# Kernel optimization log

Measured on AMD Instinct MI355X. Metric: run time of the kernel, lower is better.

## Reference

```python
import jax, jax.numpy as jnp
import numpy as np

IN_FEATURES = 2048
HIDDEN_DIM = 1024
ENC_DIM = 1024
DEC_DIM = IN_FEATURES - ENC_DIM
MASK_VAL = -50000.0


def setup_inputs() -> dict:
    key = jax.random.key(0)
    k1, k2, k3, k4, k5 = jax.random.split(key, 5)
    B, S = 32, 2048
    encoder_outputs = jax.random.normal(k1, (B, S, ENC_DIM), dtype=jnp.float32)
    decoder_state = jax.random.normal(k2, (B, DEC_DIM), dtype=jnp.float32)
    # lengths in [1, S]
    sequence_length = jax.random.randint(k3, (B,), 1, S + 1).astype(jnp.int64)
    # fc_w: Linear(in_features, hidden_dim, bias=False) -> weight [hidden, in_feat]
    W = jax.random.normal(k4, (HIDDEN_DIM, IN_FEATURES), dtype=jnp.float32) / np.sqrt(IN_FEATURES)
    # fc_v: Linear(hidden_dim, 1, bias=False) -> weight [1, hidden]; store as [hidden]
    v = jax.random.normal(k5, (HIDDEN_DIM,), dtype=jnp.float32) / np.sqrt(HIDDEN_DIM)
    return {"encoder_outputs": encoder_outputs, "sequence_length": sequence_length,
            "decoder_state": decoder_state, "W": W, "v": v}


def reference(encoder_outputs, sequence_length, decoder_state, W, v):
    # score = v^T tanh(W [h; s]) == v^T tanh(W_enc h + W_dec s)  (avoids concat)
    W_enc = W[:, :ENC_DIM]      # [H, De]
    W_dec = W[:, ENC_DIM:]      # [H, Dd]
    # [B, S, H] + [B, 1, H]
    hidden = jnp.tanh(jnp.einsum('bse,he->bsh', encoder_outputs, W_enc)
                      + jnp.einsum('bd,hd->bh', decoder_state, W_dec)[:, None, :])
    logits = jnp.einsum('bsh,h->bs', hidden, v)                      # [B, S]
    S = logits.shape[1]
    mask = jnp.arange(S)[None, :] < sequence_length[:, None]          # [B, S]
    masked_logits = jnp.where(mask, logits, jnp.float32(MASK_VAL))
    attn_weight = jax.nn.softmax(masked_logits, axis=1)               # [B, S]
    out = jnp.einsum('bs,bse->be', attn_weight, encoder_outputs)      # [B, De]
    return (out, attn_weight)
```

## Files before the change

kernel.cpp:

```cpp
#include <hip/hip_runtime.h>
#include <hip/hip_bf16.h>

#define B 32
#define S 2048
#define E 1024
#define H 1024
#define MASK_VAL -50000.0f

typedef __attribute__((ext_vector_type(8))) short bf16x8_t;
typedef __attribute__((ext_vector_type(4))) float f32x4_t;

__device__ __forceinline__ float fast_tanh(float x) {
    float a = fabsf(x);
    float e = __expf(-2.0f * a);
    float t = (1.0f - e) / (1.0f + e);
    return copysignf(t, x);
}

__device__ __forceinline__ float b2f(short s) {
    return __uint_as_float(((unsigned)(unsigned short)s) << 16);
}

__device__ __forceinline__ bf16x8_t cvt8(const float4 f0, const float4 f1) {
    union { bf16x8_t s8; __hip_bfloat162 h[4]; } u;
    u.h[0] = __float22bfloat162_rn(make_float2(f0.x, f0.y));
    u.h[1] = __float22bfloat162_rn(make_float2(f0.z, f0.w));
    u.h[2] = __float22bfloat162_rn(make_float2(f1.x, f1.y));
    u.h[3] = __float22bfloat162_rn(make_float2(f1.z, f1.w));
    return u.s8;
}

__device__ __forceinline__ void gload16(const void* g, void* l) {
    __builtin_amdgcn_global_load_lds(
        (const __attribute__((address_space(1))) void*)g,
        (__attribute__((address_space(3))) void*)l, 16, 0, 0);
}

__global__ __launch_bounds__(256) void kprep(
    const float* __restrict__ W, const float* __restrict__ dec,
    __hip_bfloat16* __restrict__ Wb, float* __restrict__ dec_proj)
{
    int blk = blockIdx.x, tid = threadIdx.x;
    if (blk < 1024) {
        int idx = (blk * 256 + tid) * 4;
        int h = idx >> 10, e = idx & 1023;
        float4 f = *(const float4*)(W + (size_t)h * 2048 + e);
        __hip_bfloat162 p0 = __float22bfloat162_rn(make_float2(f.x, f.y));
        __hip_bfloat162 p1 = __float22bfloat162_rn(make_float2(f.z, f.w));
        *reinterpret_cast<__hip_bfloat162*>(Wb + idx)     = p0;
        *reinterpret_cast<__hip_bfloat162*>(Wb + idx + 2) = p1;
    } else {
        int gid = (blk - 1024) * 256 + tid;
        int b = gid >> 10, h = gid & 1023;
        const float4* wd = (const float4*)(W + (size_t)h * 2048 + 1024);
        const float4* dd = (const float4*)(dec + b * 1024);
        float acc = 0.f;
        for (int d = 0; d < 256; ++d) {
            float4 w4 = wd[d], d4 = dd[d];
            acc += w4.x * d4.x + w4.y * d4.y + w4.z * d4.z + w4.w * d4.w;
        }
        dec_proj[gid] = acc;
    }
}

__global__ __launch_bounds__(256) void k0_encconv(
    const float* __restrict__ enc, const int* __restrict__ seq,
    __hip_bfloat16* __restrict__ encb)
{
    int c = blockIdx.x, b = blockIdx.y;
    if (c * 128 >= seq[b]) return;
    size_t base = ((size_t)b * S + c * 128) * E;
    const float* src = enc + base;
    __hip_bfloat16* dst = encb + base;
    int tid = threadIdx.x;
    #pragma unroll 4
    for (int it = 0; it < 64; ++it) {
        int idx = it * 2048 + tid * 8;
        float4 f0 = *(const float4*)(src + idx);
        float4 f1 = *(const float4*)(src + idx + 4);
        *(bf16x8_t*)(dst + idx) = cvt8(f0, f1);
    }
}

template<int AMODE>
__global__ __launch_bounds__(256, 2) void k2_mfma(
    const float* __restrict__ enc, const __hip_bfloat16* __restrict__ encb,
    const __hip_bfloat16* __restrict__ Wb, const float* __restrict__ v,
    const float* __restrict__ dec_proj, const int* __restrict__ seq,
    float* __restrict__ part)
{
    const int bid  = blockIdx.x;
    const int pair = (bid >> 6) * 8 + (bid & 7);
    const int ht   = (bid >> 3) & 7;
    const int b    = pair >> 4;
    const int s0   = (pair & 15) * 128;
    if (s0 >= seq[b]) return;
    const int h0 = ht * 128;

    const int tid  = threadIdx.x;
    const int wave = tid >> 6;
    const int lane = tid & 63;
    const int wr = wave >> 1, wc = wave & 1;
    const int cr = lane & 15, cg = lane >> 4;

    __shared__ __hip_bfloat16 Al[2][128 * 64];
    __shared__ __hip_bfloat16 Bl[2][128 * 64];

    const int colb  = (tid & 7) * 16;
    const int rbase = tid >> 3;

    f32x4_t acc[4][4];
    #pragma unroll
    for (int m = 0; m < 4; ++m)
        #pragma unroll
        for (int n = 0; n < 4; ++n)
            acc[m][n] = (f32x4_t){0.f, 0.f, 0.f, 0.f};

    auto stage = [&](int buf, int kt) {
        #pragma unroll
        for (int i = 0; i < 4; ++i) {
            const int row   = i * 32 + rbase;
            const int scolb = colb ^ ((row & 7) << 4);
            const __hip_bfloat16* bg =
                Wb + (((size_t)(h0 + row)) << 10) + kt * 64 + (scolb >> 1);
            gload16(bg, (char*)&Bl[buf][0] + (i * 256 + tid) * 16);
            if (AMODE == 0) {
                const __hip_bfloat16* ag =
                    encb + (((size_t)b * S + s0 + row) << 10) + kt * 64 + (scolb >> 1);
                gload16(ag, (char*)&Al[buf][0] + (i * 256 + tid) * 16);
            } else {
                const float* af =
                    enc + (((size_t)b * S + s0 + row) << 10) + kt * 64 + (tid & 7) * 8;
                bf16x8_t v8 = cvt8(*(const float4*)af, *(const float4*)(af + 4));
                *(bf16x8_t*)((char*)&Al[buf][0] + row * 128 + scolb) = v8;
            }
        }
    };

    stage(0, 0);
    __syncthreads();
    int cur = 0;
    for (int kt = 0; kt < 16; ++kt) {
        if (kt < 15) stage(cur ^ 1, kt + 1);
        bf16x8_t afr[2][4], bfr[2][4];
        #pragma unroll
        for (int ks = 0; ks < 2; ++ks) {
            #pragma unroll
            for (int m = 0; m < 4; ++m) {
                const int arow  = wr * 64 + m * 16 + cr;
                const int acolb = (ks * 64 + cg * 16) ^ ((arow & 7) << 4);
                afr[ks][m] = *(const bf16x8_t*)((const char*)&Al[cur][0] + arow * 128 + acolb);
                const int brow  = wc * 64 + m * 16 + cr;
                const int bcolb = (ks * 64 + cg * 16) ^ ((brow & 7) << 4);
                bfr[ks][m] = *(const bf16x8_t*)((const char*)&Bl[cur][0] + brow * 128 + bcolb);
            }
        }
        #pragma unroll
        for (int ks = 0; ks < 2; ++ks)
            #pragma unroll
            for (int m = 0; m < 4; ++m)
                #pragma unroll
                for (int n = 0; n < 4; ++n)
                    acc[m][n] = __builtin_amdgcn_mfma_f32_16x16x32_bf16(
                        afr[ks][m], bfr[ks][n], acc[m][n], 0, 0, 0);
        __syncthreads();
        cur ^= 1;
    }

    float vv[4], dp[4];
    #pragma unroll
    for (int n = 0; n < 4; ++n) {
        int h = h0 + wc * 64 + n * 16 + cr;
        vv[n] = v[h];
        dp[n] = dec_proj[b * H + h];
    }
    #pragma unroll
    for (int m = 0; m < 4; ++m) {
        #pragma unroll
        for (int j = 0; j < 4; ++j) {
            float t = 0.f;
            #pragma unroll
            for (int n = 0; n < 4; ++n)
                t += vv[n] * fast_tanh(acc[m][n][j] + dp[n]);
            t += __shfl_xor(t, 1);
            t += __shfl_xor(t, 2);
            t += __shfl_xor(t, 4);
            t += __shfl_xor(t, 8);
            if (cr == 0) {
                int srow = s0 + wr * 64 + m * 16 + cg * 4 + j;
                part[(size_t)(b * S + srow) * 16 + ht * 2 + wc] = t;
            }
        }
    }
}

__global__ __launch_bounds__(256) void k3_softmax(
    const float* __restrict__ part, const int* __restrict__ seq,
    float* __restrict__ attn)
{
    int b = blockIdx.x, tid = threadIdx.x;
    int len = seq[b];
    float vals[8];
    float mx = -3.4e38f;
    #pragma unroll
    for (int i = 0; i < 8; ++i) {
        int s = i * 256 + tid;
        float x = MASK_VAL;
        if (s < len) {
            const f32x4_t* p = (const f32x4_t*)&part[(size_t)(b * S + s) * 16];
            f32x4_t a = p[0], c = p[1], d = p[2], e = p[3];
            x = (a[0] + a[1] + a[2] + a[3]) + (c[0] + c[1] + c[2] + c[3]) +
                (d[0] + d[1] + d[2] + d[3]) + (e[0] + e[1] + e[2] + e[3]);
        }
        vals[i] = x;
        mx = fmaxf(mx, x);
    }
    #pragma unroll
    for (int off = 1; off < 64; off <<= 1) mx = fmaxf(mx, __shfl_xor(mx, off));
    __shared__ float red[8];
    int wave = tid >> 6, lane = tid & 63;
    if (lane == 0) red[wave] = mx;
    __syncthreads();
    mx = fmaxf(fmaxf(red[0], red[1]), fmaxf(red[2], red[3]));
    float e[8];
    float sum = 0.f;
    #pragma unroll
    for (int i = 0; i < 8; ++i) { e[i] = __expf(vals[i] - mx); sum += e[i]; }
    #pragma unroll
    for (int off = 1; off < 64; off <<= 1) sum += __shfl_xor(sum, off);
    if (lane == 0) red[4 + wave] = sum;
    __syncthreads();
    sum = red[4] + red[5] + red[6] + red[7];
    float inv = 1.0f / sum;
    #pragma unroll
    for (int i = 0; i < 8; ++i) attn[b * S + i * 256 + tid] = e[i] * inv;
}

template<int AMODE>
__global__ __launch_bounds__(256) void k4_partial(
    const float* __restrict__ enc, const __hip_bfloat16* __restrict__ encb,
    const float* __restrict__ attn, const int* __restrict__ seq,
    float* __restrict__ opart)
{
    int c = blockIdx.x, b = blockIdx.y, tid = threadIdx.x;
    int base_s = c * 256;
    int len = seq[b];
    if (AMODE == 0) {
        int e0 = (tid & 127) * 8;
        int so = tid >> 7;
        float av[8];
        #pragma unroll
        for (int j = 0; j < 8; ++j) av[j] = 0.f;
        if (base_s < len) {
            int s_end = min(256, len - base_s);
            for (int s = so; s < s_end; s += 2) {
                float w = attn[b * S + base_s + s];
                bf16x8_t u = *(const bf16x8_t*)(encb +
                    (((size_t)b * S + base_s + s) << 10) + e0);
                #pragma unroll
                for (int j = 0; j < 8; ++j) av[j] += w * b2f(u[j]);
            }
        }
        float* dst = opart + (((size_t)(b * 8 + c) * 2 + so) << 10) + e0;
        *(float4*)dst       = make_float4(av[0], av[1], av[2], av[3]);
        *(float4*)(dst + 4) = make_float4(av[4], av[5], av[6], av[7]);
    } else {
        float4 acc = make_float4(0.f, 0.f, 0.f, 0.f);
        if (base_s < len) {
            int s_end = min(256, len - base_s);
            const float* ep = enc + ((size_t)b * S + base_s) * E + (tid & 255) * 4;
            const float* ap = attn + b * S + base_s;
            for (int s = 0; s < s_end; ++s) {
                float w = ap[s];
                float4 ev = *(const float4*)ep;
                ep += E;
                acc.x += w * ev.x; acc.y += w * ev.y;
                acc.z += w * ev.z; acc.w += w * ev.w;
            }
        }
        float* dst = opart + (((size_t)(b * 8 + c) * 2) << 10) + tid * 4;
        *(float4*)dst = acc;
        float* dst2 = opart + (((size_t)(b * 8 + c) * 2 + 1) << 10) + tid * 4;
        *(float4*)dst2 = make_float4(0.f, 0.f, 0.f, 0.f);
    }
}

__global__ __launch_bounds__(256) void k5_reduce(
    const float* __restrict__ opart, float* __restrict__ out)
{
    int gid = blockIdx.x * 256 + threadIdx.x;
    int b = gid >> 10, e = gid & 1023;
    float s = 0.f;
    #pragma unroll
    for (int c = 0; c < 16; ++c) s += opart[((size_t)(b * 16 + c) << 10) + e];
    out[gid] = s;
}

extern "C" void kernel_launch(void* const* d_in, const int* in_sizes, int n_in,
                              void* d_out, int out_size, void* d_ws, size_t ws_size,
                              hipStream_t stream)
{
    const float* enc = (const float*)d_in[0];
    const int*   seq = (const int*)d_in[1];
    const float* dec = (const float*)d_in[2];
    const float* W   = (const float*)d_in[3];
    const float* v   = (const float*)d_in[4];

    float* out  = (float*)d_out;
    float* attn = out + B * E;

    float* dec_proj = (float*)d_ws;
    float* part     = dec_proj + B * H;
    float* opart    = part + (size_t)B * S * 16;
    __hip_bfloat16* Wb = (__hip_bfloat16*)(opart + (size_t)B * 16 * 1024);
    __hip_bfloat16* encb = Wb + (size_t)H * E;

    const size_t need = (size_t)(B * H + B * S * 16 + B * 16 * 1024) * 4
                      + (size_t)H * E * 2 + (size_t)B * S * E * 2;
    const bool use_encb = ws_size >= need;

    hipLaunchKernelGGL(kprep, dim3(1024 + 128), dim3(256), 0, stream,
                       W, dec, Wb, dec_proj);
    if (use_encb) {
        hipLaunchKernelGGL(k0_encconv, dim3(S / 128, B), dim3(256), 0, stream,
                           enc, seq, encb);
        hipLaunchKernelGGL(k2_mfma<0>, dim3(4096), dim3(256), 0, stream,
                           enc, encb, Wb, v, dec_proj, seq, part);
    } else {
        hipLaunchKernelGGL(k2_mfma<1>, dim3(4096), dim3(256), 0, stream,
                           enc, encb, Wb, v, dec_proj, seq, part);
    }
    hipLaunchKernelGGL(k3_softmax, dim3(B), dim3(256), 0, stream,
                       part, seq, attn);
    if (use_encb) {
        hipLaunchKernelGGL(k4_partial<0>, dim3(8, B), dim3(256), 0, stream,
                           enc, encb, attn, seq, opart);
    } else {
        hipLaunchKernelGGL(k4_partial<1>, dim3(8, B), dim3(256), 0, stream,
                           enc, encb, attn, seq, opart);
    }
    hipLaunchKernelGGL(k5_reduce, dim3(B * E / 256), dim3(256), 0, stream,
                       opart, out);
}
```

Before: 265.2 us.

## Enlarge MFMA score tile to 256x256 with 512 threads and fuse enc conversion into prep

The score GEMM moves from 128x128 tiles with 256 threads to 256x256 tiles with 512 threads (8 waves, each computing 128x64). This raises operand reuse per LDS load and cuts global traffic for W and enc. The enc-to-bf16 conversion kernel is folded into the prep kernel to save a launch. In exchange, LDS use doubles to 128KB per block, accumulator register pressure rises, and the coarser 256-row sequence granularity skips fewer masked rows.

```diff
diff --git a/kernel.cpp b/kernel.cpp
--- a/kernel.cpp
+++ b/kernel.cpp
@@ -38,7 +38,9 @@
 
 __global__ __launch_bounds__(256) void kprep(
     const float* __restrict__ W, const float* __restrict__ dec,
-    __hip_bfloat16* __restrict__ Wb, float* __restrict__ dec_proj)
+    const float* __restrict__ enc, const int* __restrict__ seq,
+    __hip_bfloat16* __restrict__ Wb, float* __restrict__ dec_proj,
+    __hip_bfloat16* __restrict__ encb)
 {
     int blk = blockIdx.x, tid = threadIdx.x;
     if (blk < 1024) {
@@ -49,7 +51,7 @@
         __hip_bfloat162 p1 = __float22bfloat162_rn(make_float2(f.z, f.w));
         *reinterpret_cast<__hip_bfloat162*>(Wb + idx)     = p0;
         *reinterpret_cast<__hip_bfloat162*>(Wb + idx + 2) = p1;
-    } else {
+    } else if (blk < 1152) {
         int gid = (blk - 1024) * 256 + tid;
         int b = gid >> 10, h = gid & 1023;
         const float4* wd = (const float4*)(W + (size_t)h * 2048 + 1024);
@@ -60,58 +62,56 @@
             acc += w4.x * d4.x + w4.y * d4.y + w4.z * d4.z + w4.w * d4.w;
         }
         dec_proj[gid] = acc;
-    }
-}
-
-__global__ __launch_bounds__(256) void k0_encconv(
-    const float* __restrict__ enc, const int* __restrict__ seq,
-    __hip_bfloat16* __restrict__ encb)
-{
-    int c = blockIdx.x, b = blockIdx.y;
-    if (c * 128 >= seq[b]) return;
-    size_t base = ((size_t)b * S + c * 128) * E;
-    const float* src = enc + base;
-    __hip_bfloat16* dst = encb + base;
-    int tid = threadIdx.x;
-    #pragma unroll 4
-    for (int it = 0; it < 64; ++it) {
-        int idx = it * 2048 + tid * 8;
-        float4 f0 = *(const float4*)(src + idx);
-        float4 f1 = *(const float4*)(src + idx + 4);
-        *(bf16x8_t*)(dst + idx) = cvt8(f0, f1);
+    } else {
+        int g = blk - 1152;
+        int c = g & 15, b = g >> 4;
+        if (c * 128 >= seq[b]) return;
+        size_t base = ((size_t)b * S + c * 128) * E;
+        const float* src = enc + base;
+        __hip_bfloat16* dst = encb + base;
+        #pragma unroll 4
+        for (int it = 0; it < 64; ++it) {
+            int idx = it * 2048 + tid * 8;
+            float4 f0 = *(const float4*)(src + idx);
+            float4 f1 = *(const float4*)(src + idx + 4);
+            *(bf16x8_t*)(dst + idx) = cvt8(f0, f1);
+        }
     }
 }
 
 template<int AMODE>
-__global__ __launch_bounds__(256, 2) void k2_mfma(
+__global__ __launch_bounds__(512, 2) void k2_mfma(
     const float* __restrict__ enc, const __hip_bfloat16* __restrict__ encb,
     const __hip_bfloat16* __restrict__ Wb, const float* __restrict__ v,
     const float* __restrict__ dec_proj, const int* __restrict__ seq,
     float* __restrict__ part)
 {
-    const int bid  = blockIdx.x;
-    const int pair = (bid >> 6) * 8 + (bid & 7);
-    const int ht   = (bid >> 3) & 7;
-    const int b    = pair >> 4;
-    const int s0   = (pair & 15) * 128;
+    const int bid = blockIdx.x;
+    const int xcd = bid & 7;
+    const int q   = bid >> 3;
+    const int nt  = q & 3;
+    const int p   = (q >> 2) * 8 + xcd;
+    const int b   = p >> 3;
+    const int st  = p & 7;
+    const int s0  = st * 256;
     if (s0 >= seq[b]) return;
-    const int h0 = ht * 128;
+    const int h0 = nt * 256;
 
     const int tid  = threadIdx.x;
     const int wave = tid >> 6;
     const int lane = tid & 63;
-    const int wr = wave >> 1, wc = wave & 1;
+    const int wr = wave >> 2, wc = wave & 3;
     const int cr = lane & 15, cg = lane >> 4;
 
-    __shared__ __hip_bfloat16 Al[2][128 * 64];
-    __shared__ __hip_bfloat16 Bl[2][128 * 64];
+    __shared__ __hip_bfloat16 Al[2][256 * 64];
+    __shared__ __hip_bfloat16 Bl[2][256 * 64];
 
     const int colb  = (tid & 7) * 16;
     const int rbase = tid >> 3;
 
-    f32x4_t acc[4][4];
-    #pragma unroll
-    for (int m = 0; m < 4; ++m)
+    f32x4_t acc[8][4];
+    #pragma unroll
+    for (int m = 0; m < 8; ++m)
         #pragma unroll
         for (int n = 0; n < 4; ++n)
             acc[m][n] = (f32x4_t){0.f, 0.f, 0.f, 0.f};
@@ -119,15 +119,15 @@
     auto stage = [&](int buf, int kt) {
         #pragma unroll
         for (int i = 0; i < 4; ++i) {
-            const int row   = i * 32 + rbase;
+            const int row   = i * 64 + rbase;
             const int scolb = colb ^ ((row & 7) << 4);
             const __hip_bfloat16* bg =
                 Wb + (((size_t)(h0 + row)) << 10) + kt * 64 + (scolb >> 1);
-            gload16(bg, (char*)&Bl[buf][0] + (i * 256 + tid) * 16);
+            gload16(bg, (char*)&Bl[buf][0] + (i * 512 + tid) * 16);
             if (AMODE == 0) {
                 const __hip_bfloat16* ag =
                     encb + (((size_t)b * S + s0 + row) << 10) + kt * 64 + (scolb >> 1);
-                gload16(ag, (char*)&Al[buf][0] + (i * 256 + tid) * 16);
+                gload16(ag, (char*)&Al[buf][0] + (i * 512 + tid) * 16);
             } else {
                 const float* af =
                     enc + (((size_t)b * S + s0 + row) << 10) + kt * 64 + (tid & 7) * 8;
@@ -142,27 +142,28 @@
     int cur = 0;
     for (int kt = 0; kt < 16; ++kt) {
         if (kt < 15) stage(cur ^ 1, kt + 1);
-        bf16x8_t afr[2][4], bfr[2][4];
         #pragma unroll
         for (int ks = 0; ks < 2; ++ks) {
+            bf16x8_t afr[8], bfr[4];
             #pragma unroll
-            for (int m = 0; m < 4; ++m) {
-                const int arow  = wr * 64 + m * 16 + cr;
+            for (int m = 0; m < 8; ++m) {
+                const int arow  = wr * 128 + m * 16 + cr;
                 const int acolb = (ks * 64 + cg * 16) ^ ((arow & 7) << 4);
-                afr[ks][m] = *(const bf16x8_t*)((const char*)&Al[cur][0] + arow * 128 + acolb);
-                const int brow  = wc * 64 + m * 16 + cr;
+                afr[m] = *(const bf16x8_t*)((const char*)&Al[cur][0] + arow * 128 + acolb);
+            }
+            #pragma unroll
+            for (int n = 0; n < 4; ++n) {
+                const int brow  = wc * 64 + n * 16 + cr;
                 const int bcolb = (ks * 64 + cg * 16) ^ ((brow & 7) << 4);
-                bfr[ks][m] = *(const bf16x8_t*)((const char*)&Bl[cur][0] + brow * 128 + bcolb);
-            }
-        }
-        #pragma unroll
-        for (int ks = 0; ks < 2; ++ks)
+                bfr[n] = *(const bf16x8_t*)((const char*)&Bl[cur][0] + brow * 128 + bcolb);
+            }
             #pragma unroll
-            for (int m = 0; m < 4; ++m)
+            for (int m = 0; m < 8; ++m)
                 #pragma unroll
                 for (int n = 0; n < 4; ++n)
                     acc[m][n] = __builtin_amdgcn_mfma_f32_16x16x32_bf16(
-                        afr[ks][m], bfr[ks][n], acc[m][n], 0, 0, 0);
+                        afr[m], bfr[n], acc[m][n], 0, 0, 0);
+        }
         __syncthreads();
         cur ^= 1;
     }
@@ -175,7 +176,7 @@
         dp[n] = dec_proj[b * H + h];
     }
     #pragma unroll
-    for (int m = 0; m < 4; ++m) {
+    for (int m = 0; m < 8; ++m) {
         #pragma unroll
         for (int j = 0; j < 4; ++j) {
             float t = 0.f;
@@ -187,8 +188,8 @@
             t += __shfl_xor(t, 4);
             t += __shfl_xor(t, 8);
             if (cr == 0) {
-                int srow = s0 + wr * 64 + m * 16 + cg * 4 + j;
-                part[(size_t)(b * S + srow) * 16 + ht * 2 + wc] = t;
+                int srow = s0 + wr * 128 + m * 16 + cg * 4 + j;
+                part[(size_t)(b * S + srow) * 16 + nt * 4 + wc] = t;
             }
         }
     }
@@ -319,15 +320,15 @@
                       + (size_t)H * E * 2 + (size_t)B * S * E * 2;
     const bool use_encb = ws_size >= need;
 
-    hipLaunchKernelGGL(kprep, dim3(1024 + 128), dim3(256), 0, stream,
-                       W, dec, Wb, dec_proj);
     if (use_encb) {
-        hipLaunchKernelGGL(k0_encconv, dim3(S / 128, B), dim3(256), 0, stream,
-                           enc, seq, encb);
-        hipLaunchKernelGGL(k2_mfma<0>, dim3(4096), dim3(256), 0, stream,
+        hipLaunchKernelGGL(kprep, dim3(1664), dim3(256), 0, stream,
+                           W, dec, enc, seq, Wb, dec_proj, encb);
+        hipLaunchKernelGGL(k2_mfma<0>, dim3(1024), dim3(512), 0, stream,
                            enc, encb, Wb, v, dec_proj, seq, part);
     } else {
-        hipLaunchKernelGGL(k2_mfma<1>, dim3(4096), dim3(256), 0, stream,
+        hipLaunchKernelGGL(kprep, dim3(1152), dim3(256), 0, stream,
+                           W, dec, enc, seq, Wb, dec_proj, encb);
+        hipLaunchKernelGGL(k2_mfma<1>, dim3(1024), dim3(512), 0, stream,
                            enc, encb, Wb, v, dec_proj, seq, part);
     }
     hipLaunchKernelGGL(k3_softmax, dim3(B), dim3(256), 0, stream,
```

New measurement: 305.8 us. 15.3% more time.

## Fuse encoder bf16 conversion into first hidden-tile GEMM pass; rebalance prep and partial kernels

Applied to the files above, without the earlier changes.

The standalone fp32-to-bf16 encoder conversion kernel is removed. A first GEMM launch, covering hidden tile 0, converts encoder tiles on the fly and writes the bf16 copy as a side effect. A second launch then covers the remaining seven hidden tiles from the bf16 copy, which saves one full pass over the fp32 encoder. The decoder projection now runs one block per hidden row, with the weight row cached in LDS and a shuffle reduction. The attention-weighted sum uses 128-row chunks, giving twice as many blocks, at the cost of a larger partial buffer and a longer final reduction.

```diff
diff --git a/kernel.cpp b/kernel.cpp
--- a/kernel.cpp
+++ b/kernel.cpp
@@ -50,50 +50,45 @@
         *reinterpret_cast<__hip_bfloat162*>(Wb + idx)     = p0;
         *reinterpret_cast<__hip_bfloat162*>(Wb + idx + 2) = p1;
     } else {
-        int gid = (blk - 1024) * 256 + tid;
-        int b = gid >> 10, h = gid & 1023;
-        const float4* wd = (const float4*)(W + (size_t)h * 2048 + 1024);
-        const float4* dd = (const float4*)(dec + b * 1024);
+        int h = blk - 1024;
+        __shared__ float4 wlds[256];
+        wlds[tid] = *(const float4*)(W + (size_t)h * 2048 + 1024 + tid * 4);
+        __syncthreads();
+        int b = tid >> 3, chunk = tid & 7;
+        const float4* dd = (const float4*)(dec + b * 1024 + chunk * 128);
         float acc = 0.f;
-        for (int d = 0; d < 256; ++d) {
-            float4 w4 = wd[d], d4 = dd[d];
+        #pragma unroll
+        for (int i = 0; i < 32; ++i) {
+            float4 w4 = wlds[chunk * 32 + i];
+            float4 d4 = dd[i];
             acc += w4.x * d4.x + w4.y * d4.y + w4.z * d4.z + w4.w * d4.w;
         }
-        dec_proj[gid] = acc;
-    }
-}
-
-__global__ __launch_bounds__(256) void k0_encconv(
-    const float* __restrict__ enc, const int* __restrict__ seq,
-    __hip_bfloat16* __restrict__ encb)
-{
-    int c = blockIdx.x, b = blockIdx.y;
-    if (c * 128 >= seq[b]) return;
-    size_t base = ((size_t)b * S + c * 128) * E;
-    const float* src = enc + base;
-    __hip_bfloat16* dst = encb + base;
-    int tid = threadIdx.x;
-    #pragma unroll 4
-    for (int it = 0; it < 64; ++it) {
-        int idx = it * 2048 + tid * 8;
-        float4 f0 = *(const float4*)(src + idx);
-        float4 f1 = *(const float4*)(src + idx + 4);
-        *(bf16x8_t*)(dst + idx) = cvt8(f0, f1);
-    }
-}
-
-template<int AMODE>
+        acc += __shfl_xor(acc, 1);
+        acc += __shfl_xor(acc, 2);
+        acc += __shfl_xor(acc, 4);
+        if (chunk == 0) dec_proj[b * H + h] = acc;
+    }
+}
+
+template<int MODE>
 __global__ __launch_bounds__(256, 2) void k2_mfma(
-    const float* __restrict__ enc, const __hip_bfloat16* __restrict__ encb,
+    const float* __restrict__ enc, __hip_bfloat16* __restrict__ encb,
     const __hip_bfloat16* __restrict__ Wb, const float* __restrict__ v,
     const float* __restrict__ dec_proj, const int* __restrict__ seq,
     float* __restrict__ part)
 {
-    const int bid  = blockIdx.x;
-    const int pair = (bid >> 6) * 8 + (bid & 7);
-    const int ht   = (bid >> 3) & 7;
-    const int b    = pair >> 4;
-    const int s0   = (pair & 15) * 128;
+    const int bid = blockIdx.x;
+    int pair, ht;
+    if (MODE == 1) {
+        pair = bid; ht = 0;
+    } else if (MODE == 0) {
+        const int xcd = bid & 7, j = bid >> 3;
+        pair = (j / 7) * 8 + xcd; ht = j % 7 + 1;
+    } else {
+        pair = (bid >> 6) * 8 + (bid & 7); ht = (bid >> 3) & 7;
+    }
+    const int b  = pair >> 4;
+    const int s0 = (pair & 15) * 128;
     if (s0 >= seq[b]) return;
     const int h0 = ht * 128;
 
@@ -124,15 +119,18 @@
             const __hip_bfloat16* bg =
                 Wb + (((size_t)(h0 + row)) << 10) + kt * 64 + (scolb >> 1);
             gload16(bg, (char*)&Bl[buf][0] + (i * 256 + tid) * 16);
-            if (AMODE == 0) {
+            if (MODE == 0) {
                 const __hip_bfloat16* ag =
                     encb + (((size_t)b * S + s0 + row) << 10) + kt * 64 + (scolb >> 1);
                 gload16(ag, (char*)&Al[buf][0] + (i * 256 + tid) * 16);
             } else {
-                const float* af =
-                    enc + (((size_t)b * S + s0 + row) << 10) + kt * 64 + (tid & 7) * 8;
+                const size_t aoff = (((size_t)b * S + s0 + row) << 10)
+                                  + kt * 64 + (tid & 7) * 8;
+                const float* af = enc + aoff;
                 bf16x8_t v8 = cvt8(*(const float4*)af, *(const float4*)(af + 4));
                 *(bf16x8_t*)((char*)&Al[buf][0] + row * 128 + scolb) = v8;
+                if (MODE == 1)
+                    *(bf16x8_t*)(encb + aoff) = v8;
             }
         }
     };
@@ -243,7 +241,7 @@
     float* __restrict__ opart)
 {
     int c = blockIdx.x, b = blockIdx.y, tid = threadIdx.x;
-    int base_s = c * 256;
+    int base_s = c * 128;
     int len = seq[b];
     if (AMODE == 0) {
         int e0 = (tid & 127) * 8;
@@ -252,7 +250,7 @@
         #pragma unroll
         for (int j = 0; j < 8; ++j) av[j] = 0.f;
         if (base_s < len) {
-            int s_end = min(256, len - base_s);
+            int s_end = min(128, len - base_s);
             for (int s = so; s < s_end; s += 2) {
                 float w = attn[b * S + base_s + s];
                 bf16x8_t u = *(const bf16x8_t*)(encb +
@@ -261,14 +259,14 @@
                 for (int j = 0; j < 8; ++j) av[j] += w * b2f(u[j]);
             }
         }
-        float* dst = opart + (((size_t)(b * 8 + c) * 2 + so) << 10) + e0;
+        float* dst = opart + (((size_t)(b * 16 + c) * 2 + so) << 10) + e0;
         *(float4*)dst       = make_float4(av[0], av[1], av[2], av[3]);
         *(float4*)(dst + 4) = make_float4(av[4], av[5], av[6], av[7]);
     } else {
         float4 acc = make_float4(0.f, 0.f, 0.f, 0.f);
         if (base_s < len) {
-            int s_end = min(256, len - base_s);
-            const float* ep = enc + ((size_t)b * S + base_s) * E + (tid & 255) * 4;
+            int s_end = min(128, len - base_s);
+            const float* ep = enc + (((size_t)b * S + base_s) << 10) + tid * 4;
             const float* ap = attn + b * S + base_s;
             for (int s = 0; s < s_end; ++s) {
                 float w = ap[s];
@@ -278,9 +276,9 @@
                 acc.z += w * ev.z; acc.w += w * ev.w;
             }
         }
-        float* dst = opart + (((size_t)(b * 8 + c) * 2) << 10) + tid * 4;
+        float* dst = opart + (((size_t)(b * 16 + c) * 2) << 10) + tid * 4;
         *(float4*)dst = acc;
-        float* dst2 = opart + (((size_t)(b * 8 + c) * 2 + 1) << 10) + tid * 4;
+        float* dst2 = opart + (((size_t)(b * 16 + c) * 2 + 1) << 10) + tid * 4;
         *(float4*)dst2 = make_float4(0.f, 0.f, 0.f, 0.f);
     }
 }
@@ -292,7 +290,7 @@
     int b = gid >> 10, e = gid & 1023;
     float s = 0.f;
     #pragma unroll
-    for (int c = 0; c < 16; ++c) s += opart[((size_t)(b * 16 + c) << 10) + e];
+    for (int c = 0; c < 32; ++c) s += opart[((size_t)(b * 32 + c) << 10) + e];
     out[gid] = s;
 }
 
@@ -312,31 +310,31 @@
     float* dec_proj = (float*)d_ws;
     float* part     = dec_proj + B * H;
     float* opart    = part + (size_t)B * S * 16;
-    __hip_bfloat16* Wb = (__hip_bfloat16*)(opart + (size_t)B * 16 * 1024);
+    __hip_bfloat16* Wb = (__hip_bfloat16*)(opart + (size_t)B * 32 * 1024);
     __hip_bfloat16* encb = Wb + (size_t)H * E;
 
-    const size_t need = (size_t)(B * H + B * S * 16 + B * 16 * 1024) * 4
+    const size_t need = (size_t)(B * H + B * S * 16 + B * 32 * 1024) * 4
                       + (size_t)H * E * 2 + (size_t)B * S * E * 2;
     const bool use_encb = ws_size >= need;
 
-    hipLaunchKernelGGL(kprep, dim3(1024 + 128), dim3(256), 0, stream,
+    hipLaunchKernelGGL(kprep, dim3(2048), dim3(256), 0, stream,
                        W, dec, Wb, dec_proj);
     if (use_encb) {
-        hipLaunchKernelGGL(k0_encconv, dim3(S / 128, B), dim3(256), 0, stream,
-                           enc, seq, encb);
-        hipLaunchKernelGGL(k2_mfma<0>, dim3(4096), dim3(256), 0, stream,
+        hipLaunchKernelGGL(k2_mfma<1>, dim3(512), dim3(256), 0, stream,
                            enc, encb, Wb, v, dec_proj, seq, part);
-    } else {
-        hipLaunchKernelGGL(k2_mfma<1>, dim3(4096), dim3(256), 0, stream,
+        hipLaunchKernelGGL(k2_mfma<0>, dim3(3584), dim3(256), 0, stream,
+                           enc, encb, Wb, v, dec_proj, seq, part);
+    } else {
+        hipLaunchKernelGGL(k2_mfma<2>, dim3(4096), dim3(256), 0, stream,
                            enc, encb, Wb, v, dec_proj, seq, part);
     }
     hipLaunchKernelGGL(k3_softmax, dim3(B), dim3(256), 0, stream,
                        part, seq, attn);
     if (use_encb) {
-        hipLaunchKernelGGL(k4_partial<0>, dim3(8, B), dim3(256), 0, stream,
+        hipLaunchKernelGGL(k4_partial<0>, dim3(16, B), dim3(256), 0, stream,
                            enc, encb, attn, seq, opart);
     } else {
-        hipLaunchKernelGGL(k4_partial<1>, dim3(8, B), dim3(256), 0, stream,
+        hipLaunchKernelGGL(k4_partial<1>, dim3(16, B), dim3(256), 0, stream,
                            enc, encb, attn, seq, opart);
     }
     hipLaunchKernelGGL(k5_reduce, dim3(B * E / 256), dim3(256), 0, stream,
```

Measured after the change: 245.6 us. -7.4%, faster.
